# Performance work log

Measured on AMD Instinct MI355X. Metric: run time of the kernel, lower is better.

Reference implementation:

```python
import jax, jax.numpy as jnp
import numpy as np

B, N, E = 128, 16384, 1048576
H, C = 512, 10


def setup_inputs() -> dict:
    key = jax.random.key(0)
    ks = jax.random.split(key, 10)
    x = jax.random.normal(ks[0], (B, N), dtype=jnp.float32)
    edge_index = jax.random.randint(ks[1], (2, E), 0, N, dtype=jnp.int64)
    edge_weight = jax.random.uniform(ks[2], (E,), dtype=jnp.float32)
    W1 = jax.random.normal(ks[3], (H, N), dtype=jnp.float32) * (1.0 / np.sqrt(N))
    b1 = jax.random.normal(ks[4], (H,), dtype=jnp.float32) * 0.01
    W2 = jax.random.normal(ks[5], (H, H), dtype=jnp.float32) * (1.0 / np.sqrt(H))
    b2 = jax.random.normal(ks[6], (H,), dtype=jnp.float32) * 0.01
    Wfc = jax.random.normal(ks[7], (C, H), dtype=jnp.float32) * (1.0 / np.sqrt(H))
    bfc = jax.random.normal(ks[8], (C,), dtype=jnp.float32) * 0.01
    return {"x": x, "edge_index": edge_index, "edge_weight": edge_weight,
            "W1": W1, "b1": b1, "W2": W2, "b2": b2, "Wfc": Wfc, "bfc": bfc}


def _sgconv_propagate(x, edge_index, edge_weight):
    """One GCN-normalized propagation (SGConv K=1, lin.weight==1, no bias).
    Batched edge offsets in the original == same operator applied per row.
    x: (B, N); edge_index: (2, E); edge_weight: (E,). Returns (B, N).
    """
    n = x.shape[1]
    src, dst = edge_index[0], edge_index[1]
    loop = jnp.arange(n, dtype=src.dtype)
    src_f = jnp.concatenate([src, loop])
    dst_f = jnp.concatenate([dst, loop])
    w_f = jnp.concatenate([edge_weight, jnp.ones((n,), x.dtype)])  # self-loop weight 1
    deg = jax.ops.segment_sum(w_f, dst_f, num_segments=n)  # in-degree (col)
    dinv = jnp.where(deg > 0, jax.lax.rsqrt(jnp.maximum(deg, 1e-12)), 0.0)
    norm = dinv[src_f] * w_f * dinv[dst_f]  # (E+N,)
    msgs = x[:, src_f] * norm  # (B, E+N) gather + scale
    return jax.ops.segment_sum(msgs.T, dst_f, num_segments=n).T  # scatter-add -> (B, N)


def reference(x, edge_index, edge_weight, W1, b1, W2, b2, Wfc, bfc):
    h = _sgconv_propagate(x, edge_index, edge_weight)  # diffusion (B, N)
    h = jax.nn.relu(h @ W1.T + b1)  # Linear(N->H) + ReLU
    h = jax.nn.relu(h @ W2.T + b2)  # Linear(H->H) + ReLU
    return h @ Wfc.T + bfc  # fc (H->C), softmax=False, dropout=0 (eval)
```

## Files before the change

kernel.cpp:

```cpp
#include <hip/hip_runtime.h>
#include <hip/hip_bf16.h>
#include <stdint.h>

#define B_DIM 128
#define N_DIM 16384
#define E_DIM 1048576
#define H_DIM 512
#define C_DIM 10
#define NWG 256
#define CHUNK (E_DIM / NWG)
#define NWORD8 (N_DIM / 4)
#define NGRP 8
#define WPG (NWG / NGRP)
#define SPLITK 64
#define KC (N_DIM / SPLITK)

typedef __attribute__((ext_vector_type(8))) short short8;
typedef __attribute__((ext_vector_type(4))) float f32x4;

__device__ __forceinline__ uint32_t f2bf(float f) {
    uint32_t u = __float_as_uint(f);
    return (u + 0x7fffu + ((u >> 16) & 1u)) >> 16;
}

__global__ void __launch_bounds__(256) k_thist(const float* __restrict__ x,
                                               uint16_t* __restrict__ xTh,
                                               const int* __restrict__ dst,
                                               uint32_t* __restrict__ slab) {
    __shared__ uint32_t ls[NWORD8];
    int bid = blockIdx.x, t = threadIdx.x;
    {
        float* ftile = (float*)ls;
        int tx = t & 31, tyb = t >> 5;
        for (int tile = bid * 8; tile < bid * 8 + 8; tile++) {
            int bx = tile >> 2, by = tile & 3;
#pragma unroll
            for (int r = 0; r < 4; r++) {
                int ty = r * 8 + tyb;
                ftile[ty * 33 + tx] = x[(size_t)(by * 32 + ty) * N_DIM + bx * 32 + tx];
            }
            __syncthreads();
#pragma unroll
            for (int r = 0; r < 4; r++) {
                int ty = r * 8 + tyb;
                xTh[(size_t)(bx * 32 + ty) * B_DIM + by * 32 + tx] =
                    (uint16_t)f2bf(ftile[tx * 33 + ty]);
            }
            __syncthreads();
        }
    }
#pragma unroll
    for (int i = 0; i < NWORD8 / 256; i++) ls[i * 256 + t] = 0;
    __syncthreads();
#pragma unroll
    for (int i = 0; i < CHUNK / 256; i++) {
        int d = dst[bid * CHUNK + i * 256 + t];
        atomicAdd(&ls[d >> 2], 1u << ((d & 3) << 3));
    }
    __syncthreads();
#pragma unroll
    for (int i = 0; i < NWORD8 / 256; i++)
        slab[(size_t)bid * NWORD8 + i * 256 + t] = ls[i * 256 + t];
}

__global__ void __launch_bounds__(128) k_scanA8(uint32_t* __restrict__ slab,
                                                uint32_t* __restrict__ grp) {
    int b = blockIdx.x;
    int g = b >> 5;
    int j = (b & 31) * 128 + threadIdx.x;
    uint32_t run = 0;
    for (int w = g * WPG; w < (g + 1) * WPG; w++) {
        uint32_t c = slab[(size_t)w * NWORD8 + j];
        slab[(size_t)w * NWORD8 + j] = run;
        run += c;
    }
    grp[(size_t)g * NWORD8 + j] = run;
}

__global__ void __launch_bounds__(1024) k_scanBC8(uint32_t* __restrict__ grp,
                                                  int* __restrict__ offs) {
    __shared__ uint32_t part[1024];
    int t = threadIdx.x;
    uint32_t tw[4];
    int loc[16];
    uint32_t s = 0;
    int k = 0;
#pragma unroll
    for (int i = 0; i < 4; i++) {
        int j = t * 4 + i;
        uint32_t run = 0;
#pragma unroll
        for (int g = 0; g < NGRP; g++) {
            uint32_t c = grp[(size_t)g * NWORD8 + j];
            grp[(size_t)g * NWORD8 + j] = run;
            run += c;
        }
        tw[i] = run;
#pragma unroll
        for (int b4 = 0; b4 < 4; b4++) {
            loc[k] = (int)s;
            s += (tw[i] >> (b4 * 8)) & 0xffu;
            k++;
        }
    }
    part[t] = s;
    __syncthreads();
    for (int off = 1; off < 1024; off <<= 1) {
        uint32_t v = (t >= off) ? part[t - off] : 0;
        __syncthreads();
        part[t] += v;
        __syncthreads();
    }
    uint32_t ex = (t == 0) ? 0 : part[t - 1];
#pragma unroll
    for (int i = 0; i < 16; i++) offs[t * 16 + i] = (int)(ex + loc[i]);
    if (t == 1023) offs[N_DIM] = (int)part[1023];
}

__global__ void __launch_bounds__(256) k_place2(const int* __restrict__ src,
                                                const int* __restrict__ dst,
                                                const float* __restrict__ ew,
                                                const uint32_t* __restrict__ slab,
                                                const uint32_t* __restrict__ grp,
                                                const int* __restrict__ offs,
                                                int2* __restrict__ packed) {
    __shared__ uint32_t cur[N_DIM];
    int w = blockIdx.x, t = threadIdx.x;
    int g = w >> 5;
#pragma unroll
    for (int i = 0; i < NWORD8 / 256; i++) {
        int j = i * 256 + t;
        uint32_t pv = slab[(size_t)w * NWORD8 + j];
        uint32_t gv = grp[(size_t)g * NWORD8 + j];
        int4 o = *(const int4*)&offs[4 * j];
        cur[4 * j + 0] = (uint32_t)o.x + (gv & 0xffu) + (pv & 0xffu);
        cur[4 * j + 1] = (uint32_t)o.y + ((gv >> 8) & 0xffu) + ((pv >> 8) & 0xffu);
        cur[4 * j + 2] = (uint32_t)o.z + ((gv >> 16) & 0xffu) + ((pv >> 16) & 0xffu);
        cur[4 * j + 3] = (uint32_t)o.w + (gv >> 24) + (pv >> 24);
    }
    __syncthreads();
    int e = w * CHUNK + t;
    int s = src[e], d = dst[e];
    float wv = ew[e];
#pragma unroll
    for (int i = 0; i < CHUNK / 256; i++) {
        int sn = 0, dn = 0;
        float wn = 0.f;
        if (i + 1 < CHUNK / 256) {
            int en = e + 256;
            sn = src[en]; dn = dst[en]; wn = ew[en];
        }
        uint32_t pos = atomicAdd(&cur[d], 1u);
        packed[pos] = make_int2(s, __float_as_int(wv));
        s = sn; d = dn; wv = wn; e += 256;
    }
}

__global__ void __launch_bounds__(256) k_deg(const int* __restrict__ offs,
                                             const int2* __restrict__ packed,
                                             float* __restrict__ dinv) {
    int d = blockIdx.x * 4 + (threadIdx.x >> 6);
    int lane = threadIdx.x & 63;
    int e0 = offs[d], e1 = offs[d + 1];
    float s = 0.f;
    for (int e = e0 + lane; e < e1; e += 64)
        s += __int_as_float(packed[e].y);
#pragma unroll
    for (int o = 32; o > 0; o >>= 1) s += __shfl_down(s, o);
    if (lane == 0) dinv[d] = rsqrtf(s + 1.0f);
}

__global__ void __launch_bounds__(256) k_diffuse(const uint16_t* __restrict__ xTh,
                                                 const int* __restrict__ offs,
                                                 const int2* __restrict__ packed,
                                                 const float* __restrict__ dinv,
                                                 uint16_t* __restrict__ hB) {
    __shared__ uint4 ls[128];
    int wave = threadIdx.x >> 6;
    int d0 = blockIdx.x * 8 + wave * 2;
    int lane = threadIdx.x & 63;
    int g = lane >> 4;
    int colh = lane & 15;
    const uint4* x4 = (const uint4*)xTh;
    int oA = offs[d0], oM = offs[d0 + 1], oB = offs[d0 + 2];
    int eA = oA + lane;
    int2 pA = (eA < oM) ? packed[eA] : make_int2(0, 0);
    int eB = oM + lane;
    int2 pB = (eB < oB) ? packed[eB] : make_int2(0, 0);
    pA.y = __float_as_int(__int_as_float(pA.y) * dinv[pA.x]);
    pB.y = __float_as_int(__int_as_float(pB.y) * dinv[pB.x]);
    float accA[8], accB[8];
#pragma unroll
    for (int k = 0; k < 8; k++) { accA[k] = 0.f; accB[k] = 0.f; }
    for (int base = oA; base < oM; base += 64) {
        int2 pc = pA;
        int en = base + 64 + lane;
        pA = (en < oM) ? packed[en] : make_int2(0, 0);
        pA.y = __float_as_int(__int_as_float(pA.y) * dinv[pA.x]);
#pragma unroll
        for (int i = 0; i < 64; i += 4) {
            int idx = i + g;
            int sx = __shfl(pc.x, idx);
            float nm = __shfl(__int_as_float(pc.y), idx);
            uint4 xs = x4[(size_t)sx * 16 + colh];
            accA[0] = fmaf(nm, __uint_as_float(xs.x << 16), accA[0]);
            accA[1] = fmaf(nm, __uint_as_float(xs.x & 0xffff0000u), accA[1]);
            accA[2] = fmaf(nm, __uint_as_float(xs.y << 16), accA[2]);
            accA[3] = fmaf(nm, __uint_as_float(xs.y & 0xffff0000u), accA[3]);
            accA[4] = fmaf(nm, __uint_as_float(xs.z << 16), accA[4]);
            accA[5] = fmaf(nm, __uint_as_float(xs.z & 0xffff0000u), accA[5]);
            accA[6] = fmaf(nm, __uint_as_float(xs.w << 16), accA[6]);
            accA[7] = fmaf(nm, __uint_as_float(xs.w & 0xffff0000u), accA[7]);
        }
    }
    for (int base = oM; base < oB; base += 64) {
        int2 pc = pB;
        int en = base + 64 + lane;
        pB = (en < oB) ? packed[en] : make_int2(0, 0);
        pB.y = __float_as_int(__int_as_float(pB.y) * dinv[pB.x]);
#pragma unroll
        for (int i = 0; i < 64; i += 4) {
            int idx = i + g;
            int sx = __shfl(pc.x, idx);
            float nm = __shfl(__int_as_float(pc.y), idx);
            uint4 xs = x4[(size_t)sx * 16 + colh];
            accB[0] = fmaf(nm, __uint_as_float(xs.x << 16), accB[0]);
            accB[1] = fmaf(nm, __uint_as_float(xs.x & 0xffff0000u), accB[1]);
            accB[2] = fmaf(nm, __uint_as_float(xs.y << 16), accB[2]);
            accB[3] = fmaf(nm, __uint_as_float(xs.y & 0xffff0000u), accB[3]);
            accB[4] = fmaf(nm, __uint_as_float(xs.z << 16), accB[4]);
            accB[5] = fmaf(nm, __uint_as_float(xs.z & 0xffff0000u), accB[5]);
            accB[6] = fmaf(nm, __uint_as_float(xs.w << 16), accB[6]);
            accB[7] = fmaf(nm, __uint_as_float(xs.w & 0xffff0000u), accB[7]);
        }
    }
#pragma unroll
    for (int off = 16; off <= 32; off <<= 1)
#pragma unroll
        for (int k = 0; k < 8; k++) {
            accA[k] += __shfl_xor(accA[k], off);
            accB[k] += __shfl_xor(accB[k], off);
        }
    int who = lane >> 4;
    if (who < 2) {
        int dd = d0 + who;
        float dv = dinv[dd];
        uint4 sv = x4[(size_t)dd * 16 + colh];
        float o[8];
#pragma unroll
        for (int k = 0; k < 8; k++) o[k] = (who == 0) ? accA[k] : accB[k];
        o[0] = (o[0] + dv * __uint_as_float(sv.x << 16)) * dv;
        o[1] = (o[1] + dv * __uint_as_float(sv.x & 0xffff0000u)) * dv;
        o[2] = (o[2] + dv * __uint_as_float(sv.y << 16)) * dv;
        o[3] = (o[3] + dv * __uint_as_float(sv.y & 0xffff0000u)) * dv;
        o[4] = (o[4] + dv * __uint_as_float(sv.z << 16)) * dv;
        o[5] = (o[5] + dv * __uint_as_float(sv.z & 0xffff0000u)) * dv;
        o[6] = (o[6] + dv * __uint_as_float(sv.w << 16)) * dv;
        o[7] = (o[7] + dv * __uint_as_float(sv.w & 0xffff0000u)) * dv;
        uint4 r;
        r.x = f2bf(o[0]) | (f2bf(o[1]) << 16);
        r.y = f2bf(o[2]) | (f2bf(o[3]) << 16);
        r.z = f2bf(o[4]) | (f2bf(o[5]) << 16);
        r.w = f2bf(o[6]) | (f2bf(o[7]) << 16);
        ls[(wave * 2 + who) * 16 + colh] = r;
    }
    __syncthreads();
    int t = threadIdx.x;
    if (t < 128) {
        const uint16_t* l16 = (const uint16_t*)ls;
        uint16_t v0 = l16[0 * 128 + t], v1 = l16[1 * 128 + t];
        uint16_t v2 = l16[2 * 128 + t], v3 = l16[3 * 128 + t];
        uint16_t v4 = l16[4 * 128 + t], v5 = l16[5 * 128 + t];
        uint16_t v6 = l16[6 * 128 + t], v7 = l16[7 * 128 + t];
        uint4 r;
        r.x = (uint32_t)v0 | ((uint32_t)v1 << 16);
        r.y = (uint32_t)v2 | ((uint32_t)v3 << 16);
        r.z = (uint32_t)v4 | ((uint32_t)v5 << 16);
        r.w = (uint32_t)v6 | ((uint32_t)v7 << 16);
        *(uint4*)&hB[(size_t)t * N_DIM + blockIdx.x * 8] = r;
    }
}

__global__ void __launch_bounds__(256) k_gemm1(const float* __restrict__ W1,
                                               const uint16_t* __restrict__ hB,
                                               float* __restrict__ part) {
    int kc = blockIdx.x;
    int mt = blockIdx.y;
    int t = threadIdx.x, w = t >> 6, l = t & 63;
    int lr = l & 15;
    int lk = (l >> 4) * 8;
    int row = mt * 64 + w * 16 + lr;
    int k0 = kc * KC;
    f32x4 acc[8] = {};
    const float* wbase = W1 + (size_t)row * N_DIM + k0 + lk;
    const uint16_t* hbase = hB + k0 + lk;
#pragma unroll 2
    for (int ks = 0; ks < KC; ks += 32) {
        float4 wa = *(const float4*)(wbase + ks);
        float4 wb = *(const float4*)(wbase + ks + 4);
        short8 bf[8];
#pragma unroll
        for (int c = 0; c < 8; c++)
            bf[c] = *(const short8*)(hbase + (size_t)(c * 16 + lr) * N_DIM + ks);
        float wv0 = wa.x, wv1 = wa.y, wv2 = wa.z, wv3 = wa.w;
        float wv4 = wb.x, wv5 = wb.y, wv6 = wb.z, wv7 = wb.w;
        short8 ahi, alo;
        uint32_t h0;
        h0 = f2bf(wv0); ahi[0] = (short)h0; alo[0] = (short)f2bf(wv0 - __uint_as_float(h0 << 16));
        h0 = f2bf(wv1); ahi[1] = (short)h0; alo[1] = (short)f2bf(wv1 - __uint_as_float(h0 << 16));
        h0 = f2bf(wv2); ahi[2] = (short)h0; alo[2] = (short)f2bf(wv2 - __uint_as_float(h0 << 16));
        h0 = f2bf(wv3); ahi[3] = (short)h0; alo[3] = (short)f2bf(wv3 - __uint_as_float(h0 << 16));
        h0 = f2bf(wv4); ahi[4] = (short)h0; alo[4] = (short)f2bf(wv4 - __uint_as_float(h0 << 16));
        h0 = f2bf(wv5); ahi[5] = (short)h0; alo[5] = (short)f2bf(wv5 - __uint_as_float(h0 << 16));
        h0 = f2bf(wv6); ahi[6] = (short)h0; alo[6] = (short)f2bf(wv6 - __uint_as_float(h0 << 16));
        h0 = f2bf(wv7); ahi[7] = (short)h0; alo[7] = (short)f2bf(wv7 - __uint_as_float(h0 << 16));
#pragma unroll
        for (int c = 0; c < 8; c++) {
            acc[c] = __builtin_amdgcn_mfma_f32_16x16x32_bf16(ahi, bf[c], acc[c], 0, 0, 0);
            acc[c] = __builtin_amdgcn_mfma_f32_16x16x32_bf16(alo, bf[c], acc[c], 0, 0, 0);
        }
    }
    float* pbase = part + (size_t)kc * (H_DIM * B_DIM)
                 + (size_t)(mt * 64 + w * 16 + (l >> 4) * 4) * B_DIM + lr;
#pragma unroll
    for (int c = 0; c < 8; c++)
#pragma unroll
        for (int r = 0; r < 4; r++)
            pbase[(size_t)r * B_DIM + c * 16] = acc[c][r];
}

__global__ void __launch_bounds__(256) k_reduce1(const float* __restrict__ part,
                                                 const float* __restrict__ b1,
                                                 float* __restrict__ h1) {
    __shared__ float ls[128][9];
    int bid = blockIdx.x;
    int t = threadIdx.x;
    int j0 = bid * 8;
    int jl = t >> 5;
    int b0 = (t & 31) * 4;
    float bias = b1[j0 + jl];
    float4 s = make_float4(bias, bias, bias, bias);
    const float* pb = part + (size_t)j0 * B_DIM + t * 4;
#pragma unroll
    for (int c = 0; c < SPLITK; c++) {
        float4 v = *(const float4*)(pb + (size_t)c * (H_DIM * B_DIM));
        s.x += v.x; s.y += v.y; s.z += v.z; s.w += v.w;
    }
    ls[b0 + 0][jl] = fmaxf(s.x, 0.f);
    ls[b0 + 1][jl] = fmaxf(s.y, 0.f);
    ls[b0 + 2][jl] = fmaxf(s.z, 0.f);
    ls[b0 + 3][jl] = fmaxf(s.w, 0.f);
    __syncthreads();
    int b = t >> 1;
    int off = (t & 1) * 4;
    float4 w = make_float4(ls[b][off], ls[b][off + 1], ls[b][off + 2], ls[b][off + 3]);
    *(float4*)&h1[(size_t)b * H_DIM + j0 + off] = w;
}

__global__ void __launch_bounds__(1024) k_tail23(const float* __restrict__ W2,
                                                 const float* __restrict__ b2,
                                                 const float* __restrict__ Wfc,
                                                 const float* __restrict__ bfc,
                                                 const float* __restrict__ h1,
                                                 float* __restrict__ out) {
    __shared__ float h2s[H_DIM];
    int b = blockIdx.x;
    int t = threadIdx.x;
    int w = t >> 6;
    int l = t & 63;
    const float* hb = h1 + (size_t)b * H_DIM;
    float hv[8];
#pragma unroll
    for (int k = 0; k < 8; k++) hv[k] = hb[k * 64 + l];
#pragma unroll
    for (int it = 0; it < 4; it++) {
        int j0 = w * 32 + it * 8;
        float outv = 0.f;
#pragma unroll
        for (int jj = 0; jj < 8; jj++) {
            const float* wrow = W2 + (size_t)(j0 + jj) * H_DIM;
            float a = 0.f;
#pragma unroll
            for (int k = 0; k < 8; k++) a = fmaf(wrow[k * 64 + l], hv[k], a);
#pragma unroll
            for (int o = 1; o < 64; o <<= 1) a += __shfl_xor(a, o);
            if (l == jj) outv = a;
        }
        if (l < 8) h2s[j0 + l] = fmaxf(outv + b2[j0 + l], 0.f);
    }
    __syncthreads();
    if (w == 0) {
        float hv2[8];
#pragma unroll
        for (int k = 0; k < 8; k++) hv2[k] = h2s[k * 64 + l];
        float outv = 0.f;
#pragma unroll
        for (int c = 0; c < C_DIM; c++) {
            const float* wrow = Wfc + (size_t)c * H_DIM;
            float a = 0.f;
#pragma unroll
            for (int k = 0; k < 8; k++) a = fmaf(wrow[k * 64 + l], hv2[k], a);
#pragma unroll
            for (int o = 1; o < 64; o <<= 1) a += __shfl_xor(a, o);
            if (l == c) outv = a;
        }
        if (l < C_DIM) out[b * C_DIM + l] = outv + bfc[l];
    }
}

extern "C" void kernel_launch(void* const* d_in, const int* in_sizes, int n_in,
                              void* d_out, int out_size, void* d_ws, size_t ws_size,
                              hipStream_t stream) {
    const float* x   = (const float*)d_in[0];
    const int*   ei  = (const int*)d_in[1];
    const float* ew  = (const float*)d_in[2];
    const float* W1  = (const float*)d_in[3];
    const float* b1  = (const float*)d_in[4];
    const float* W2  = (const float*)d_in[5];
    const float* b2  = (const float*)d_in[6];
    const float* Wfc = (const float*)d_in[7];
    const float* bfc = (const float*)d_in[8];
    float* out = (float*)d_out;

    const int* src = ei;
    const int* dst = ei + E_DIM;

    char* ws = (char*)d_ws;
    size_t off = 0;
    auto alloc = [&](size_t bytes) -> void* {
        void* p = ws + off;
        off = (off + bytes + 255) & ~(size_t)255;
        return p;
    };
    uint16_t* xTh = (uint16_t*)alloc((size_t)N_DIM * B_DIM * 2);
    int2*  packed = (int2*) alloc((size_t)E_DIM * 8);
    size_t sort_bytes = (size_t)NWG * NWORD8 * 4 + (size_t)NGRP * NWORD8 * 4;
    size_t part_bytes = (size_t)SPLITK * H_DIM * B_DIM * 4;
    char* scratch = (char*)alloc(sort_bytes > part_bytes ? sort_bytes : part_bytes);
    float* h1     = (float*)alloc((size_t)H_DIM * B_DIM * 4);
    int*   offs   = (int*)  alloc((size_t)(N_DIM + 1) * 4);
    float* dinv   = (float*)alloc((size_t)N_DIM * 4);
    uint16_t* hB  = (uint16_t*)alloc((size_t)B_DIM * N_DIM * 2);
    uint32_t* slab = (uint32_t*)scratch;
    uint32_t* grp  = (uint32_t*)(scratch + (size_t)NWG * NWORD8 * 4);
    float* part    = (float*)scratch;
    if (off > ws_size) return;

    k_thist<<<NWG, 256, 0, stream>>>(x, xTh, dst, slab);
    k_scanA8<<<NWG, 128, 0, stream>>>(slab, grp);
    k_scanBC8<<<1, 1024, 0, stream>>>(grp, offs);
    k_place2<<<NWG, 256, 0, stream>>>(src, dst, ew, slab, grp, offs, packed);
    k_deg<<<N_DIM / 4, 256, 0, stream>>>(offs, packed, dinv);
    k_diffuse<<<N_DIM / 8, 256, 0, stream>>>(xTh, offs, packed, dinv, hB);
    k_gemm1<<<dim3(SPLITK, H_DIM / 64), 256, 0, stream>>>(W1, hB, part);
    k_reduce1<<<64, 256, 0, stream>>>(part, b1, h1);
    k_tail23<<<B_DIM, 1024, 0, stream>>>(W2, b2, Wfc, bfc, h1, out);
}
```

Baseline: 124.9 us.

## Prescale transposed x rows by source dinv in degree kernel

```diff
diff --git a/kernel.cpp b/kernel.cpp
--- a/kernel.cpp
+++ b/kernel.cpp
@@ -24,7 +24,7 @@
 }
 
 __global__ void __launch_bounds__(256) k_thist(const float* __restrict__ x,
-                                               uint16_t* __restrict__ xTh,
+                                               float* __restrict__ xT,
                                                const int* __restrict__ dst,
                                                uint32_t* __restrict__ slab) {
     __shared__ uint32_t ls[NWORD8];
@@ -43,8 +43,7 @@
 #pragma unroll
             for (int r = 0; r < 4; r++) {
                 int ty = r * 8 + tyb;
-                xTh[(size_t)(bx * 32 + ty) * B_DIM + by * 32 + tx] =
-                    (uint16_t)f2bf(ftile[tx * 33 + ty]);
+                xT[(size_t)(bx * 32 + ty) * B_DIM + by * 32 + tx] = ftile[tx * 33 + ty];
             }
             __syncthreads();
         }
@@ -156,9 +155,11 @@
     }
 }
 
-__global__ void __launch_bounds__(256) k_deg(const int* __restrict__ offs,
-                                             const int2* __restrict__ packed,
-                                             float* __restrict__ dinv) {
+__global__ void __launch_bounds__(256) k_degscale(const int* __restrict__ offs,
+                                                  const int2* __restrict__ packed,
+                                                  float* __restrict__ dinv,
+                                                  const float* __restrict__ xT,
+                                                  uint16_t* __restrict__ xTh) {
     int d = blockIdx.x * 4 + (threadIdx.x >> 6);
     int lane = threadIdx.x & 63;
     int e0 = offs[d], e1 = offs[d + 1];
@@ -167,7 +168,11 @@
         s += __int_as_float(packed[e].y);
 #pragma unroll
     for (int o = 32; o > 0; o >>= 1) s += __shfl_down(s, o);
-    if (lane == 0) dinv[d] = rsqrtf(s + 1.0f);
+    float dv = __shfl(rsqrtf(s + 1.0f), 0);
+    if (lane == 0) dinv[d] = dv;
+    float2 v = ((const float2*)&xT[(size_t)d * B_DIM])[lane];
+    uint32_t b = f2bf(v.x * dv) | (f2bf(v.y * dv) << 16);
+    ((uint32_t*)(xTh + (size_t)d * B_DIM))[lane] = b;
 }
 
 __global__ void __launch_bounds__(256) k_diffuse(const uint16_t* __restrict__ xTh,
@@ -187,8 +192,6 @@
     int2 pA = (eA < oM) ? packed[eA] : make_int2(0, 0);
     int eB = oM + lane;
     int2 pB = (eB < oB) ? packed[eB] : make_int2(0, 0);
-    pA.y = __float_as_int(__int_as_float(pA.y) * dinv[pA.x]);
-    pB.y = __float_as_int(__int_as_float(pB.y) * dinv[pB.x]);
     float accA[8], accB[8];
 #pragma unroll
     for (int k = 0; k < 8; k++) { accA[k] = 0.f; accB[k] = 0.f; }
@@ -196,7 +199,6 @@
         int2 pc = pA;
         int en = base + 64 + lane;
         pA = (en < oM) ? packed[en] : make_int2(0, 0);
-        pA.y = __float_as_int(__int_as_float(pA.y) * dinv[pA.x]);
 #pragma unroll
         for (int i = 0; i < 64; i += 4) {
             int idx = i + g;
@@ -217,7 +219,6 @@
         int2 pc = pB;
         int en = base + 64 + lane;
         pB = (en < oB) ? packed[en] : make_int2(0, 0);
-        pB.y = __float_as_int(__int_as_float(pB.y) * dinv[pB.x]);
 #pragma unroll
         for (int i = 0; i < 64; i += 4) {
             int idx = i + g;
@@ -249,14 +250,14 @@
         float o[8];
 #pragma unroll
         for (int k = 0; k < 8; k++) o[k] = (who == 0) ? accA[k] : accB[k];
-        o[0] = (o[0] + dv * __uint_as_float(sv.x << 16)) * dv;
-        o[1] = (o[1] + dv * __uint_as_float(sv.x & 0xffff0000u)) * dv;
-        o[2] = (o[2] + dv * __uint_as_float(sv.y << 16)) * dv;
-        o[3] = (o[3] + dv * __uint_as_float(sv.y & 0xffff0000u)) * dv;
-        o[4] = (o[4] + dv * __uint_as_float(sv.z << 16)) * dv;
-        o[5] = (o[5] + dv * __uint_as_float(sv.z & 0xffff0000u)) * dv;
-        o[6] = (o[6] + dv * __uint_as_float(sv.w << 16)) * dv;
-        o[7] = (o[7] + dv * __uint_as_float(sv.w & 0xffff0000u)) * dv;
+        o[0] = (o[0] + __uint_as_float(sv.x << 16)) * dv;
+        o[1] = (o[1] + __uint_as_float(sv.x & 0xffff0000u)) * dv;
+        o[2] = (o[2] + __uint_as_float(sv.y << 16)) * dv;
+        o[3] = (o[3] + __uint_as_float(sv.y & 0xffff0000u)) * dv;
+        o[4] = (o[4] + __uint_as_float(sv.z << 16)) * dv;
+        o[5] = (o[5] + __uint_as_float(sv.z & 0xffff0000u)) * dv;
+        o[6] = (o[6] + __uint_as_float(sv.w << 16)) * dv;
+        o[7] = (o[7] + __uint_as_float(sv.w & 0xffff0000u)) * dv;
         uint4 r;
         r.x = f2bf(o[0]) | (f2bf(o[1]) << 16);
         r.y = f2bf(o[2]) | (f2bf(o[3]) << 16);
@@ -432,6 +433,7 @@
         off = (off + bytes + 255) & ~(size_t)255;
         return p;
     };
+    float* xT     = (float*)alloc((size_t)N_DIM * B_DIM * 4);
     uint16_t* xTh = (uint16_t*)alloc((size_t)N_DIM * B_DIM * 2);
     int2*  packed = (int2*) alloc((size_t)E_DIM * 8);
     size_t sort_bytes = (size_t)NWG * NWORD8 * 4 + (size_t)NGRP * NWORD8 * 4;
@@ -446,11 +448,11 @@
     float* part    = (float*)scratch;
     if (off > ws_size) return;
 
-    k_thist<<<NWG, 256, 0, stream>>>(x, xTh, dst, slab);
+    k_thist<<<NWG, 256, 0, stream>>>(x, xT, dst, slab);
     k_scanA8<<<NWG, 128, 0, stream>>>(slab, grp);
     k_scanBC8<<<1, 1024, 0, stream>>>(grp, offs);
     k_place2<<<NWG, 256, 0, stream>>>(src, dst, ew, slab, grp, offs, packed);
-    k_deg<<<N_DIM / 4, 256, 0, stream>>>(offs, packed, dinv);
+    k_degscale<<<N_DIM / 4, 256, 0, stream>>>(offs, packed, dinv, xT, xTh);
     k_diffuse<<<N_DIM / 8, 256, 0, stream>>>(xTh, offs, packed, dinv, hB);
     k_gemm1<<<dim3(SPLITK, H_DIM / 64), 256, 0, stream>>>(W1, hB, part);
     k_reduce1<<<64, 256, 0, stream>>>(part, b1, h1);
```

After: 122.6 us. No clear change (-1.8%).
